# Optimization experiments

Measured on AMD Instinct MI355X. Metric: run time of the kernel, lower is better.

## Reference

```python
import jax, jax.numpy as jnp
import numpy as np

N_NODES = 50000
N_EDGES = 800000
D_FEAT = 64


def setup_inputs() -> dict:
    key = jax.random.key(0)
    k1, k2, k3 = jax.random.split(key, 3)
    x_sum = jax.random.normal(k1, (N_NODES, D_FEAT), dtype=jnp.float32)
    x_prod = jax.random.uniform(k2, (N_NODES, D_FEAT), dtype=jnp.float32)
    edge_index = jax.random.randint(k3, (2, N_EDGES), 0, N_NODES, dtype=jnp.int64)
    return {"x_sum": x_sum, "x_prod": x_prod, "edge_index": edge_index}


def reference(x_sum, x_prod, edge_index):
    # flow='source_to_target' -> gather from edge_index[0], aggregate at edge_index[1]
    src_idx = edge_index[0]
    dst_idx = edge_index[1]
    n = x_sum.shape[0]

    # __lift__: index_select along node dim (message is identity; edge_attr/norm None)
    m_sum = x_sum[src_idx]    # [E, D]
    m_prod = x_prod[src_idx]  # [E, D]

    # scatter_sum: zeros-init + scatter_add_
    out_sum = jax.ops.segment_sum(m_sum, dst_idx, num_segments=n)

    # scatter_product: ones-init + scatter_(reduce='multiply')
    out_prod = jnp.ones((n, x_prod.shape[1]), dtype=x_prod.dtype).at[dst_idx].multiply(m_prod)

    return out_sum, out_prod
```

## Files before the change

kernel.cpp:

```cpp
#include <hip/hip_runtime.h>
#include <hip/hip_fp16.h>

#define N_NODES 50000
#define N_EDGES 800000
#define D_FEAT  64
#define BSHIFT  6
#define NBKT    782
#define PSHIFT  20
#define SRC_MASK ((1 << PSHIFT) - 1)
#define BCAP    2048

#define K1_NB    391
#define K1_TH    512
#define K1_CHUNK 2047
#define TOTSTRIDE 16

#define WS_TOT    0
#define WS_OVFC   (NBKT * TOTSTRIDE)
#define WS_PAIR   (WS_OVFC + 16)
#define WS_OVF    (WS_PAIR + NBKT * BCAP)
#define WS_PACKED (WS_OVF + 2 * N_EDGES)
#define WS_INTS   (WS_PACKED + N_NODES * D_FEAT)

__device__ inline void detect_idx_layout(const int* idx, int* flag) {
    int allzero = 1;
    #pragma unroll
    for (int i = 1; i < 129; i += 2) {
        if (idx[i] != 0) allzero = 0;
    }
    *flag = allzero;
}

__global__ __launch_bounds__(K1_TH) void front(int* __restrict__ W,
                                               const int* __restrict__ idx,
                                               const float* __restrict__ xs,
                                               const float* __restrict__ xp) {
    __shared__ int h[NBKT];
    __shared__ int flg_s;
    const int t = threadIdx.x;
    for (int i = t; i < NBKT; i += K1_TH) h[i] = 0;
    if (t == 0) flg_s = 1;
    __syncthreads();
    if (t < 128 && idx[2 * t + 1] != 0) flg_s = 0;
    __syncthreads();
    const int flg = flg_s;

    const int ebase = blockIdx.x * K1_CHUNK;
    const int eend  = min(ebase + K1_CHUNK, N_EDGES);
    int src_r[4], dst_r[4];
    #pragma unroll
    for (int i = 0; i < 4; ++i) {
        int e = ebase + t + i * K1_TH;
        bool v = (e < eend);
        int s = 0, d = 0;
        if (v) {
            if (flg) {
                s = ((const int2*)idx)[e].x;
                d = ((const int2*)idx)[N_EDGES + e].x;
            } else {
                s = idx[e];
                d = idx[N_EDGES + e];
            }
            atomicAdd(&h[d >> BSHIFT], 1);
        }
        src_r[i] = v ? s : -1;
        dst_r[i] = d;
    }

    {
        const float4* xs4 = (const float4*)xs;
        const float4* xp4 = (const float4*)xp;
        uint4* pk4 = (uint4*)(W + WS_PACKED);
        const int gtid = blockIdx.x * K1_TH + t;
        for (int g = gtid; g < (N_NODES * D_FEAT) / 4; g += K1_NB * K1_TH) {
            float4 a = xs4[g], p = xp4[g];
            union { __half2 h2; unsigned int u; } c0, c1, c2, c3;
            c0.h2 = __floats2half2_rn(a.x, p.x);
            c1.h2 = __floats2half2_rn(a.y, p.y);
            c2.h2 = __floats2half2_rn(a.z, p.z);
            c3.h2 = __floats2half2_rn(a.w, p.w);
            pk4[g] = make_uint4(c0.u, c1.u, c2.u, c3.u);
        }
    }
    __syncthreads();

    for (int j = t; j < NBKT; j += K1_TH) {
        int c = h[j];
        h[j] = (c > 0) ? atomicAdd(&W[WS_TOT + j * TOTSTRIDE], c) : 0;
    }
    __syncthreads();

    #pragma unroll
    for (int i = 0; i < 4; ++i) {
        if (src_r[i] >= 0) {
            int d = dst_r[i];
            int bkt = d >> BSHIFT;
            int pos = atomicAdd(&h[bkt], 1);
            if (pos < BCAP) {
                W[WS_PAIR + bkt * BCAP + pos] = src_r[i] | ((d & 63) << PSHIFT);
            } else {
                int op = atomicAdd(&W[WS_OVFC], 1);
                W[WS_OVF + 2 * op]     = d;
                W[WS_OVF + 2 * op + 1] = src_r[i];
            }
        }
    }
}

__global__ __launch_bounds__(512) void sort_gather(const int* __restrict__ W,
                                                   float* __restrict__ out) {
    __shared__ int pair_l[BCAP];
    __shared__ int ssrc_l[BCAP];
    __shared__ int h64[64];
    __shared__ int noff[65];
    const int b = blockIdx.x;
    const int t = threadIdx.x;
    const int nedge = min(W[WS_TOT + b * TOTSTRIDE], BCAP);
    const int pbase = WS_PAIR + b * BCAP;

    if (t < 64) h64[t] = 0;
    __syncthreads();
    for (int e = t; e < nedge; e += 512) {
        int v = W[pbase + e];
        pair_l[e] = v;
        atomicAdd(&h64[(unsigned)v >> PSHIFT], 1);
    }
    __syncthreads();
    if (t < 64) {
        int c = h64[t];
        int incl = c;
        #pragma unroll
        for (int off = 1; off < 64; off <<= 1) {
            int u = __shfl_up(incl, off, 64);
            if (t >= off) incl += u;
        }
        noff[t] = incl - c;
        if (t == 63) noff[64] = incl;
        h64[t] = incl - c;
    }
    __syncthreads();
    for (int e = t; e < nedge; e += 512) {
        int v = pair_l[e];
        int p = atomicAdd(&h64[(unsigned)v >> PSHIFT], 1);
        ssrc_l[p] = v & SRC_MASK;
    }
    __syncthreads();

    const __half2* packed = (const __half2*)(W + WS_PACKED);
    const int wave = t >> 6;
    const int lane = t & 63;
    for (int nn = wave; nn < 64; nn += 8) {
        const int node = (b << BSHIFT) + nn;
        if (node >= N_NODES) break;
        int beg = __builtin_amdgcn_readfirstlane(noff[nn]);
        int end = __builtin_amdgcn_readfirstlane(noff[nn + 1]);

        float s0 = 0.f, s1 = 0.f, s2 = 0.f, s3 = 0.f;
        float s4 = 0.f, s5 = 0.f, s6 = 0.f, s7 = 0.f;
        float p0 = 1.f, p1 = 1.f, p2 = 1.f, p3 = 1.f;
        float p4 = 1.f, p5 = 1.f, p6 = 1.f, p7 = 1.f;
        int i = beg;
        for (; i + 7 < end; i += 8) {
            int a0 = ssrc_l[i],     a1 = ssrc_l[i + 1];
            int a2 = ssrc_l[i + 2], a3 = ssrc_l[i + 3];
            int a4 = ssrc_l[i + 4], a5 = ssrc_l[i + 5];
            int a6 = ssrc_l[i + 6], a7 = ssrc_l[i + 7];
            float2 f0 = __half22float2(packed[a0 * D_FEAT + lane]);
            float2 f1 = __half22float2(packed[a1 * D_FEAT + lane]);
            float2 f2 = __half22float2(packed[a2 * D_FEAT + lane]);
            float2 f3 = __half22float2(packed[a3 * D_FEAT + lane]);
            float2 f4 = __half22float2(packed[a4 * D_FEAT + lane]);
            float2 f5 = __half22float2(packed[a5 * D_FEAT + lane]);
            float2 f6 = __half22float2(packed[a6 * D_FEAT + lane]);
            float2 f7 = __half22float2(packed[a7 * D_FEAT + lane]);
            s0 += f0.x; s1 += f1.x; s2 += f2.x; s3 += f3.x;
            s4 += f4.x; s5 += f5.x; s6 += f6.x; s7 += f7.x;
            p0 *= f0.y; p1 *= f1.y; p2 *= f2.y; p3 *= f3.y;
            p4 *= f4.y; p5 *= f5.y; p6 *= f6.y; p7 *= f7.y;
        }
        for (; i + 1 < end; i += 2) {
            int a0 = ssrc_l[i], a1 = ssrc_l[i + 1];
            float2 f0 = __half22float2(packed[a0 * D_FEAT + lane]);
            float2 f1 = __half22float2(packed[a1 * D_FEAT + lane]);
            s0 += f0.x; s1 += f1.x;
            p0 *= f0.y; p1 *= f1.y;
        }
        if (i < end) {
            float2 f = __half22float2(packed[ssrc_l[i] * D_FEAT + lane]);
            s0 += f.x;
            p0 *= f.y;
        }
        float ssum = ((s0 + s1) + (s2 + s3)) + ((s4 + s5) + (s6 + s7));
        float pprd = ((p0 * p1) * (p2 * p3)) * ((p4 * p5) * (p6 * p7));
        out[(long)node * D_FEAT + lane] = ssum;
        out[(long)N_NODES * D_FEAT + (long)node * D_FEAT + lane] = pprd;
    }

    int novf = W[WS_OVFC];
    if (novf > 0) {
        __syncthreads();
        for (int k = wave; k < novf; k += 8) {
            int d = W[WS_OVF + 2 * k];
            if ((d >> BSHIFT) == b) {
                int s = W[WS_OVF + 2 * k + 1];
                float2 f = __half22float2(packed[s * D_FEAT + lane]);
                atomicAdd(out + (long)d * D_FEAT + lane, f.x);
                unsigned int* ua =
                    (unsigned int*)(out + (long)N_NODES * D_FEAT + (long)d * D_FEAT + lane);
                unsigned int old = __hip_atomic_load(ua, __ATOMIC_RELAXED,
                                                     __HIP_MEMORY_SCOPE_AGENT);
                while (true) {
                    unsigned int assumed = old;
                    unsigned int desired =
                        __float_as_uint(__uint_as_float(assumed) * f.y);
                    old = atomicCAS(ua, assumed, desired);
                    if (old == assumed) break;
                }
            }
        }
    }
}

__device__ inline void atomicMulF32(float* addr, float val) {
    unsigned int* ua = (unsigned int*)addr;
    unsigned int old = __hip_atomic_load(ua, __ATOMIC_RELAXED, __HIP_MEMORY_SCOPE_AGENT);
    while (true) {
        unsigned int assumed = old;
        unsigned int desired = __float_as_uint(__uint_as_float(assumed) * val);
        old = atomicCAS(ua, assumed, desired);
        if (old == assumed) break;
    }
}

__global__ void fb_init(float* __restrict__ out, int* __restrict__ flag,
                        const int* __restrict__ idx) {
    const int n4 = (N_NODES * D_FEAT) / 4;
    int tid = blockIdx.x * blockDim.x + threadIdx.x;
    int stride = gridDim.x * blockDim.x;
    float4* o = (float4*)out;
    const float4 z = make_float4(0.f, 0.f, 0.f, 0.f);
    const float4 one = make_float4(1.f, 1.f, 1.f, 1.f);
    for (int i = tid; i < n4; i += stride) { o[i] = z; o[n4 + i] = one; }
    if (blockIdx.x == 0 && threadIdx.x == 0) detect_idx_layout(idx, flag);
}

__global__ void fb_scatter(const float* __restrict__ xs, const float* __restrict__ xp,
                           const int* __restrict__ idx, float* __restrict__ out,
                           const int* __restrict__ flag) {
    long tid = (long)blockIdx.x * blockDim.x + threadIdx.x;
    const long total = (long)N_EDGES * (D_FEAT / 4);
    if (tid >= total) return;
    int e = (int)(tid >> 4);
    int c = (int)(tid & 15);
    int src, dst;
    if (*flag) { src = idx[2 * e]; dst = idx[2 * (N_EDGES + e)]; }
    else       { src = idx[e];     dst = idx[N_EDGES + e]; }
    const float4 s = ((const float4*)(xs + (long)src * D_FEAT))[c];
    const float4 p = ((const float4*)(xp + (long)src * D_FEAT))[c];
    float* os = out + (long)dst * D_FEAT + c * 4;
    float* op = out + (long)N_NODES * D_FEAT + (long)dst * D_FEAT + c * 4;
    atomicAdd(os + 0, s.x); atomicAdd(os + 1, s.y);
    atomicAdd(os + 2, s.z); atomicAdd(os + 3, s.w);
    atomicMulF32(op + 0, p.x); atomicMulF32(op + 1, p.y);
    atomicMulF32(op + 2, p.z); atomicMulF32(op + 3, p.w);
}

extern "C" void kernel_launch(void* const* d_in, const int* in_sizes, int n_in,
                              void* d_out, int out_size, void* d_ws, size_t ws_size,
                              hipStream_t stream) {
    const float* x_sum  = (const float*)d_in[0];
    const float* x_prod = (const float*)d_in[1];
    const int*   eidx   = (const int*)d_in[2];
    float* out = (float*)d_out;
    int* W = (int*)d_ws;

    if (ws_size < (size_t)WS_INTS * sizeof(int)) {
        fb_init<<<1024, 256, 0, stream>>>(out, W, eidx);
        const long total = (long)N_EDGES * (D_FEAT / 4);
        int grid = (int)((total + 255) / 256);
        fb_scatter<<<grid, 256, 0, stream>>>(x_sum, x_prod, eidx, out, W);
        return;
    }

    hipMemsetAsync(W, 0, (size_t)(WS_OVFC + 16) * sizeof(int), stream);
    front<<<K1_NB, K1_TH, 0, stream>>>(W, eidx, x_sum, x_prod);
    sort_gather<<<NBKT, 512, 0, stream>>>(W, out);
}
```

Baseline: 138.1 us.

## Split gather feature columns across four blocks per bucket with edge-group lanes

The sort_gather kernel is replaced by a variant launched with four times as many blocks. Each block handles one destination bucket and one quarter of the feature columns. Within a wave, lanes split into four edge groups of 16 columns each, and partial sums and products are combined with cross-lane shuffles. The goal is more blocks and waves in flight to hide random-gather latency. The cost is that each block redoes the bucket's shared-memory counting sort, about four times the redundant work, and each gathered row segment shrinks to 64 bytes.

```diff
diff --git a/kernel.cpp b/kernel.cpp
--- a/kernel.cpp
+++ b/kernel.cpp
@@ -14,6 +14,8 @@
 #define K1_TH    512
 #define K1_CHUNK 2047
 #define TOTSTRIDE 16
+
+#define K2_NB (391 * 8)
 
 #define WS_TOT    0
 #define WS_OVFC   (NBKT * TOTSTRIDE)
@@ -107,14 +109,16 @@
     }
 }
 
-__global__ __launch_bounds__(512) void sort_gather(const int* __restrict__ W,
-                                                   float* __restrict__ out) {
+__global__ __launch_bounds__(512) void sort_gather_q(const int* __restrict__ W,
+                                                     float* __restrict__ out) {
     __shared__ int pair_l[BCAP];
     __shared__ int ssrc_l[BCAP];
     __shared__ int h64[64];
     __shared__ int noff[65];
-    const int b = blockIdx.x;
     const int t = threadIdx.x;
+    const int xslot = blockIdx.x & 7;
+    const int q = xslot >> 1;
+    const int b = ((blockIdx.x >> 3) << 1) | (xslot & 1);
     const int nedge = min(W[WS_TOT + b * TOTSTRIDE], BCAP);
     const int pbase = WS_PAIR + b * BCAP;
 
@@ -149,51 +153,47 @@
     const __half2* packed = (const __half2*)(W + WS_PACKED);
     const int wave = t >> 6;
     const int lane = t & 63;
+    const int eg   = lane >> 4;
+    const int fcol = (q << 4) + (lane & 15);
+
     for (int nn = wave; nn < 64; nn += 8) {
         const int node = (b << BSHIFT) + nn;
         if (node >= N_NODES) break;
         int beg = __builtin_amdgcn_readfirstlane(noff[nn]);
         int end = __builtin_amdgcn_readfirstlane(noff[nn + 1]);
 
-        float s0 = 0.f, s1 = 0.f, s2 = 0.f, s3 = 0.f;
-        float s4 = 0.f, s5 = 0.f, s6 = 0.f, s7 = 0.f;
-        float p0 = 1.f, p1 = 1.f, p2 = 1.f, p3 = 1.f;
-        float p4 = 1.f, p5 = 1.f, p6 = 1.f, p7 = 1.f;
+        float s0 = 0.f, s1 = 0.f, p0 = 1.f, p1 = 1.f;
         int i = beg;
         for (; i + 7 < end; i += 8) {
-            int a0 = ssrc_l[i],     a1 = ssrc_l[i + 1];
-            int a2 = ssrc_l[i + 2], a3 = ssrc_l[i + 3];
-            int a4 = ssrc_l[i + 4], a5 = ssrc_l[i + 5];
-            int a6 = ssrc_l[i + 6], a7 = ssrc_l[i + 7];
-            float2 f0 = __half22float2(packed[a0 * D_FEAT + lane]);
-            float2 f1 = __half22float2(packed[a1 * D_FEAT + lane]);
-            float2 f2 = __half22float2(packed[a2 * D_FEAT + lane]);
-            float2 f3 = __half22float2(packed[a3 * D_FEAT + lane]);
-            float2 f4 = __half22float2(packed[a4 * D_FEAT + lane]);
-            float2 f5 = __half22float2(packed[a5 * D_FEAT + lane]);
-            float2 f6 = __half22float2(packed[a6 * D_FEAT + lane]);
-            float2 f7 = __half22float2(packed[a7 * D_FEAT + lane]);
-            s0 += f0.x; s1 += f1.x; s2 += f2.x; s3 += f3.x;
-            s4 += f4.x; s5 += f5.x; s6 += f6.x; s7 += f7.x;
-            p0 *= f0.y; p1 *= f1.y; p2 *= f2.y; p3 *= f3.y;
-            p4 *= f4.y; p5 *= f5.y; p6 *= f6.y; p7 *= f7.y;
-        }
-        for (; i + 1 < end; i += 2) {
-            int a0 = ssrc_l[i], a1 = ssrc_l[i + 1];
-            float2 f0 = __half22float2(packed[a0 * D_FEAT + lane]);
-            float2 f1 = __half22float2(packed[a1 * D_FEAT + lane]);
+            int a0 = ssrc_l[i + eg];
+            int a1 = ssrc_l[i + 4 + eg];
+            float2 f0 = __half22float2(packed[a0 * D_FEAT + fcol]);
+            float2 f1 = __half22float2(packed[a1 * D_FEAT + fcol]);
             s0 += f0.x; s1 += f1.x;
             p0 *= f0.y; p1 *= f1.y;
         }
+        for (; i + 3 < end; i += 4) {
+            int a0 = ssrc_l[i + eg];
+            float2 f0 = __half22float2(packed[a0 * D_FEAT + fcol]);
+            s0 += f0.x;
+            p0 *= f0.y;
+        }
         if (i < end) {
-            float2 f = __half22float2(packed[ssrc_l[i] * D_FEAT + lane]);
-            s0 += f.x;
-            p0 *= f.y;
-        }
-        float ssum = ((s0 + s1) + (s2 + s3)) + ((s4 + s5) + (s6 + s7));
-        float pprd = ((p0 * p1) * (p2 * p3)) * ((p4 * p5) * (p6 * p7));
-        out[(long)node * D_FEAT + lane] = ssum;
-        out[(long)N_NODES * D_FEAT + (long)node * D_FEAT + lane] = pprd;
+            int e = i + eg;
+            bool v = (e < end);
+            int a = ssrc_l[v ? e : i];
+            float2 f = __half22float2(packed[a * D_FEAT + fcol]);
+            s0 += v ? f.x : 0.f;
+            p0 *= v ? f.y : 1.f;
+        }
+        float s = s0 + s1;
+        float p = p0 * p1;
+        s += __shfl_xor(s, 16, 64);  p *= __shfl_xor(p, 16, 64);
+        s += __shfl_xor(s, 32, 64);  p *= __shfl_xor(p, 32, 64);
+        if (eg == 0) {
+            out[(long)node * D_FEAT + fcol] = s;
+            out[(long)N_NODES * D_FEAT + (long)node * D_FEAT + fcol] = p;
+        }
     }
 
     int novf = W[WS_OVFC];
@@ -201,12 +201,12 @@
         __syncthreads();
         for (int k = wave; k < novf; k += 8) {
             int d = W[WS_OVF + 2 * k];
-            if ((d >> BSHIFT) == b) {
+            if ((d >> BSHIFT) == b && eg == 0) {
                 int s = W[WS_OVF + 2 * k + 1];
-                float2 f = __half22float2(packed[s * D_FEAT + lane]);
-                atomicAdd(out + (long)d * D_FEAT + lane, f.x);
+                float2 f = __half22float2(packed[s * D_FEAT + fcol]);
+                atomicAdd(out + (long)d * D_FEAT + fcol, f.x);
                 unsigned int* ua =
-                    (unsigned int*)(out + (long)N_NODES * D_FEAT + (long)d * D_FEAT + lane);
+                    (unsigned int*)(out + (long)N_NODES * D_FEAT + (long)d * D_FEAT + fcol);
                 unsigned int old = __hip_atomic_load(ua, __ATOMIC_RELAXED,
                                                      __HIP_MEMORY_SCOPE_AGENT);
                 while (true) {
@@ -284,5 +284,5 @@
 
     hipMemsetAsync(W, 0, (size_t)(WS_OVFC + 16) * sizeof(int), stream);
     front<<<K1_NB, K1_TH, 0, stream>>>(W, eidx, x_sum, x_prod);
-    sort_gather<<<NBKT, 512, 0, stream>>>(W, out);
-}
+    sort_gather_q<<<K2_NB, 512, 0, stream>>>(W, out);
+}
```

Measured after the change: 152.2 us. 10.2% more time.

## Bucket edges via shared-memory linked lists instead of two-pass atomic histogram

Applied to the files above, without the earlier changes.

Each block now threads its chunk of edges onto per-bucket linked lists in shared memory with atomicExch, storing the packed value. A thread per bucket then walks its list twice, once to count and once to write contiguously into the global bucket. This drops the second round of shared atomics and the register arrays, and makes the global writes per bucket contiguous from one thread. In exchange it adds serial pointer-chasing per bucket (about 2.6 edges each) and more shared memory per block.

```diff
diff --git a/kernel.cpp b/kernel.cpp
--- a/kernel.cpp
+++ b/kernel.cpp
@@ -35,10 +35,12 @@
                                                const int* __restrict__ idx,
                                                const float* __restrict__ xs,
                                                const float* __restrict__ xp) {
-    __shared__ int h[NBKT];
+    __shared__ int head[NBKT];
+    __shared__ int nxt[K1_CHUNK];
+    __shared__ int val[K1_CHUNK];
     __shared__ int flg_s;
     const int t = threadIdx.x;
-    for (int i = t; i < NBKT; i += K1_TH) h[i] = 0;
+    for (int i = t; i < NBKT; i += K1_TH) head[i] = -1;
     if (t == 0) flg_s = 1;
     __syncthreads();
     if (t < 128 && idx[2 * t + 1] != 0) flg_s = 0;
@@ -46,14 +48,10 @@
     const int flg = flg_s;
 
     const int ebase = blockIdx.x * K1_CHUNK;
-    const int eend  = min(ebase + K1_CHUNK, N_EDGES);
-    int src_r[4], dst_r[4];
-    #pragma unroll
-    for (int i = 0; i < 4; ++i) {
-        int e = ebase + t + i * K1_TH;
-        bool v = (e < eend);
-        int s = 0, d = 0;
-        if (v) {
+    for (int k = t; k < K1_CHUNK; k += K1_TH) {
+        int e = ebase + k;
+        if (e < N_EDGES) {
+            int s, d;
             if (flg) {
                 s = ((const int2*)idx)[e].x;
                 d = ((const int2*)idx)[N_EDGES + e].x;
@@ -61,10 +59,9 @@
                 s = idx[e];
                 d = idx[N_EDGES + e];
             }
-            atomicAdd(&h[d >> BSHIFT], 1);
-        }
-        src_r[i] = v ? s : -1;
-        dst_r[i] = d;
+            val[k] = s | ((d & 63) << PSHIFT);
+            nxt[k] = atomicExch(&head[d >> BSHIFT], k);
+        }
     }
 
     {
@@ -85,23 +82,19 @@
     __syncthreads();
 
     for (int j = t; j < NBKT; j += K1_TH) {
-        int c = h[j];
-        h[j] = (c > 0) ? atomicAdd(&W[WS_TOT + j * TOTSTRIDE], c) : 0;
-    }
-    __syncthreads();
-
-    #pragma unroll
-    for (int i = 0; i < 4; ++i) {
-        if (src_r[i] >= 0) {
-            int d = dst_r[i];
-            int bkt = d >> BSHIFT;
-            int pos = atomicAdd(&h[bkt], 1);
+        int c = 0;
+        for (int i = head[j]; i >= 0; i = nxt[i]) ++c;
+        if (c == 0) continue;
+        int base = atomicAdd(&W[WS_TOT + j * TOTSTRIDE], c);
+        int pos = base;
+        for (int i = head[j]; i >= 0; i = nxt[i], ++pos) {
+            int v = val[i];
             if (pos < BCAP) {
-                W[WS_PAIR + bkt * BCAP + pos] = src_r[i] | ((d & 63) << PSHIFT);
+                W[WS_PAIR + j * BCAP + pos] = v;
             } else {
                 int op = atomicAdd(&W[WS_OVFC], 1);
-                W[WS_OVF + 2 * op]     = d;
-                W[WS_OVF + 2 * op + 1] = src_r[i];
+                W[WS_OVF + 2 * op]     = (j << BSHIFT) | ((unsigned)v >> PSHIFT);
+                W[WS_OVF + 2 * op + 1] = v & SRC_MASK;
             }
         }
     }
```

Result: no change. 139.8 us (+1.2%).
